# Kernel optimization log

Measured on AMD Instinct MI355X. Metric: run time of the kernel, lower is better.

The kernel has to match this reference:

```python
import jax, jax.numpy as jnp
import numpy as np

B, T, D = 2, 2048, 1024
HEADS = 16
MEM = 512
HEAD_DIM = D // HEADS


def setup_inputs() -> dict:
    key = jax.random.key(0)
    k1, k2, k3, k4, k5 = jax.random.split(key, 5)
    x = jax.random.normal(k1, (B, T, D), dtype=jnp.float32)
    w_qkv = jax.random.normal(k2, (3 * D, D), dtype=jnp.float32) * (1.0 / np.sqrt(D))
    w_out = jax.random.normal(k3, (D, D), dtype=jnp.float32) * (1.0 / np.sqrt(D))
    b_out = jax.random.normal(k4, (D,), dtype=jnp.float32) * 0.01
    memory = jax.random.normal(k5, (MEM, D), dtype=jnp.float32)
    return {"x": x, "w_qkv": w_qkv, "w_out": w_out, "b_out": b_out, "memory": memory}


def reference(x, w_qkv, w_out, b_out, memory):
    b, t, d = x.shape
    h, hd = HEADS, HEAD_DIM
    scale = hd ** -0.5
    # QKV projection: [B,T,3D]
    qkv = jnp.einsum('btd,ed->bte', x, w_qkv)
    q, k, v = jnp.split(qkv, 3, axis=-1)
    # [B,H,T,hd]
    q = q.reshape(b, t, h, hd).transpose(0, 2, 1, 3)
    k = k.reshape(b, t, h, hd).transpose(0, 2, 1, 3)
    v = v.reshape(b, t, h, hd).transpose(0, 2, 1, 3)
    # memory K/V: [B,H,MEM,hd] (broadcast over batch)
    mem = memory.reshape(1, MEM, h, hd).transpose(0, 2, 1, 3)
    mem = jnp.broadcast_to(mem, (b, h, MEM, hd))
    k = jnp.concatenate([mem, k], axis=2)
    v = jnp.concatenate([mem, v], axis=2)
    # attention: scores [B,H,T,MEM+T]
    scores = jnp.einsum('bhqd,bhkd->bhqk', q, k) * scale
    weights = jax.nn.softmax(scores, axis=-1)
    out = jnp.einsum('bhqk,bhkd->bhqd', weights, v)
    out = out.transpose(0, 2, 1, 3).reshape(b, t, d)
    return jnp.einsum('btd,ed->bte', out, w_out) + b_out
```

## Files before the change

kernel.cpp:

```cpp
#include <hip/hip_runtime.h>
#include <hip/hip_bf16.h>
#include <stdint.h>

#define B_   2
#define T_   2048
#define D_   1024
#define H_   16
#define HD_  64
#define MEM_ 512
#define KV_  (MEM_ + T_)
#define NIT_ (KV_ / 64)
#define NIT2_ (NIT_ / 2)

using bf16 = __bf16;
typedef __bf16 bf16x8 __attribute__((ext_vector_type(8)));
typedef float  f32x4  __attribute__((ext_vector_type(4)));
typedef short  s16x4  __attribute__((ext_vector_type(4)));
typedef short  s16x8  __attribute__((ext_vector_type(8)));

__device__ __forceinline__ f32x4 mfma16(bf16x8 a, bf16x8 b, f32x4 c) {
  return __builtin_amdgcn_mfma_f32_16x16x32_bf16(a, b, c, 0, 0, 0);
}

__device__ __forceinline__ void gll16(const void* g, void* l) {
  __builtin_amdgcn_global_load_lds(
      (const __attribute__((address_space(1))) unsigned int*)g,
      (__attribute__((address_space(3))) unsigned int*)l, 16, 0, 0);
}

__device__ __forceinline__ unsigned short bf16_bits(float f) {
  bf16 h = (bf16)f;
  return __builtin_bit_cast(unsigned short, h);
}

__device__ __forceinline__ ushort4 pack4(f32x4 v) {
  ushort4 p;
  p.x = bf16_bits(v[0]); p.y = bf16_bits(v[1]);
  p.z = bf16_bits(v[2]); p.w = bf16_bits(v[3]);
  return p;
}

__device__ __forceinline__ bf16x8 cvt8(f32x4 a, f32x4 b) {
  bf16x8 r;
  r[0] = (bf16)a[0]; r[1] = (bf16)a[1]; r[2] = (bf16)a[2]; r[3] = (bf16)a[3];
  r[4] = (bf16)b[0]; r[5] = (bf16)b[1]; r[6] = (bf16)b[2]; r[7] = (bf16)b[3];
  return r;
}

__device__ __forceinline__ int vperm4(int u) {
  int g = u >> 4, c = (u >> 2) & 3;
  return (g >> 1) * 32 + c * 8 + (g & 1) * 4;
}

__global__ void prep(const float* __restrict__ x, const float* __restrict__ wq,
                     const float* __restrict__ memory,
                     const float* __restrict__ wout,
                     bf16* __restrict__ xb, bf16* __restrict__ wqb,
                     bf16* __restrict__ mem_k, bf16* __restrict__ mem_vt,
                     bf16* __restrict__ wob) {
  int blk = blockIdx.x;
  if (blk < 3584) {
    const float* s = (blk < 2048) ? x : wq;
    bf16* d = (blk < 2048) ? xb : wqb;
    size_t i = ((size_t)(blk < 2048 ? blk : blk - 2048) * 256 + threadIdx.x) * 8;
    f32x4 a = *(const f32x4*)(s + i);
    f32x4 b = *(const f32x4*)(s + i + 4);
    *(bf16x8*)(d + i) = cvt8(a, b);
  } else if (blk < 3840) {
    int idx8 = ((blk - 3584) * 256 + threadIdx.x) * 8;
    int m = idx8 >> 10, d0 = idx8 & 1023;
    int hh = d0 >> 6, hd0 = d0 & 63;
    f32x4 a = *(const f32x4*)(memory + idx8);
    f32x4 b = *(const f32x4*)(memory + idx8 + 4);
    *(bf16x8*)&mem_k[((size_t)hh * MEM_ + m) * HD_ + hd0] = cvt8(a, b);
  } else if (blk < 4096) {
    int idx = (blk - 3840) * 256 + threadIdx.x;
    int d = idx & 1023;
    int m0 = (idx >> 10) * 8;
    bf16x8 r;
#pragma unroll
    for (int j = 0; j < 8; j++)
      r[j] = (bf16)memory[(size_t)(m0 + j) * D_ + d];
    int u = m0 & 63;
    bf16* dst = &mem_vt[(size_t)d * MEM_ + (m0 - u) + vperm4(u)];
    s16x8 rb = __builtin_bit_cast(s16x8, r);
    *(s16x4*)dst = __builtin_shufflevector(rb, rb, 0, 1, 2, 3);
    *(s16x4*)(dst + 8) = __builtin_shufflevector(rb, rb, 4, 5, 6, 7);
  } else {
    size_t i = ((size_t)(blk - 4096) * 256 + threadIdx.x) * 8;
    f32x4 a = *(const f32x4*)(wout + i);
    f32x4 b = *(const f32x4*)(wout + i + 4);
    *(bf16x8*)(wob + i) = cvt8(a, b);
  }
}

__global__ void conv_bf16(const float* __restrict__ s, bf16* __restrict__ d) {
  size_t i = ((size_t)blockIdx.x * 256 + threadIdx.x) * 8;
  f32x4 a = *(const f32x4*)(s + i);
  f32x4 b = *(const f32x4*)(s + i + 4);
  *(bf16x8*)(d + i) = cvt8(a, b);
}

template <int EPI, bool APLANE, int NTILE>
__global__ __launch_bounds__(256, 3) void gemm_bt(
    const bf16* __restrict__ A, const bf16* __restrict__ W,
    const float* __restrict__ bias,
    bf16* __restrict__ q_ws, bf16* __restrict__ k_ws, bf16* __restrict__ vt_ws,
    float* __restrict__ Cout, int K) {
  constexpr int NF = NTILE / 32;
  constexpr int NB = NTILE / 32;
  __shared__ __align__(16) bf16 Als[128 * 64];
  __shared__ __align__(16) bf16 Bls[NTILE * 64];
  char* AB = (char*)Als;
  char* BB = (char*)Bls;
  const int nwg = gridDim.x * gridDim.y;
  int lin = blockIdx.y * gridDim.x + blockIdx.x;
  lin = (lin & 7) * (nwg >> 3) + (lin >> 3);
  const int m0 = (lin / gridDim.x) * 128;
  const int n0 = (lin % gridDim.x) * NTILE;
  const int tid = threadIdx.x;
  const int w = tid >> 6;
  const int lane = tid & 63;
  const int lx = lane & 15;
  const int quad = lane >> 4;
  const int amb = (w & 1) * 64;
  const int bnb = (w >> 1) * (NTILE / 2);
  const int srow = tid >> 3;
  const int cs = (tid & 7) ^ (srow & 7);

  f32x4 acc[4][NF];
#pragma unroll
  for (int i = 0; i < 4; i++)
#pragma unroll
    for (int j = 0; j < NF; j++) acc[i][j] = (f32x4){0.f, 0.f, 0.f, 0.f};

  for (int k0 = 0; k0 < K; k0 += 64) {
    const bf16* pa[4];
#pragma unroll
    for (int g = 0; g < 4; g++) {
      int r = srow + 32 * g;
      if constexpr (APLANE) {
        int hh = k0 >> 6, hd = cs * 8;
        int mA = m0 + r;
        pa[g] = A + ((size_t)((mA >> 11) * H_ + hh) * T_ + (mA & 2047)) * HD_ + hd;
      } else {
        pa[g] = A + (size_t)(m0 + r) * K + k0 + cs * 8;
      }
    }
    const bf16* pb[NB];
#pragma unroll
    for (int g = 0; g < NB; g++)
      pb[g] = W + (size_t)(n0 + srow + 32 * g) * K + k0 + cs * 8;

    __syncthreads();
#pragma unroll
    for (int g = 0; g < 4; g++) gll16(pa[g], AB + g * 4096 + tid * 16);
#pragma unroll
    for (int g = 0; g < NB; g++) gll16(pb[g], BB + g * 4096 + tid * 16);
    __syncthreads();

    bf16x8 af[4][2], bfr[NF][2];
    const int rk = (lx & 7) << 4;
#pragma unroll
    for (int mt = 0; mt < 4; mt++)
#pragma unroll
      for (int kh = 0; kh < 2; kh++)
        af[mt][kh] = *(const bf16x8*)(AB + (size_t)(amb + mt * 16 + lx) * 128 +
                                      ((quad * 16 + kh * 64) ^ rk));
#pragma unroll
    for (int nt = 0; nt < NF; nt++)
#pragma unroll
      for (int kh = 0; kh < 2; kh++)
        bfr[nt][kh] = *(const bf16x8*)(BB + (size_t)(bnb + nt * 16 + lx) * 128 +
                                       ((quad * 16 + kh * 64) ^ rk));
#pragma unroll
    for (int kh = 0; kh < 2; kh++)
#pragma unroll
      for (int mt = 0; mt < 4; mt++)
#pragma unroll
        for (int nt = 0; nt < NF; nt++)
          acc[mt][nt] = mfma16(af[mt][kh], bfr[nt][kh], acc[mt][nt]);
  }

  if (EPI == 0) {
#pragma unroll
    for (int mt = 0; mt < 4; mt++) {
      int mbase = m0 + amb + mt * 16 + quad * 4;
      int b = mbase >> 11;
      int t = mbase & 2047;
#pragma unroll
      for (int nt = 0; nt < NF; nt++) {
        int col = n0 + bnb + nt * 16 + lx;
        int which = col >> 10;
        int d = col & 1023;
        int hh = d >> 6, hdi = d & 63;
        int bh = b * H_ + hh;
        if (which == 0) {
#pragma unroll
          for (int r = 0; r < 4; r++)
            q_ws[((size_t)bh * T_ + t + r) * HD_ + hdi] = (bf16)acc[mt][nt][r];
        } else if (which == 1) {
#pragma unroll
          for (int r = 0; r < 4; r++)
            k_ws[((size_t)bh * T_ + t + r) * HD_ + hdi] = (bf16)acc[mt][nt][r];
        } else {
          int u = t & 63;
          *(ushort4*)&vt_ws[((size_t)bh * HD_ + hdi) * T_ + (t - u) +
                            vperm4(u)] = pack4(acc[mt][nt]);
        }
      }
    }
  } else {
#pragma unroll
    for (int nt = 0; nt < NF; nt++) {
      int col = n0 + bnb + nt * 16 + lx;
      float bias_f = bias[col];
#pragma unroll
      for (int mt = 0; mt < 4; mt++) {
        int mbase = m0 + amb + mt * 16 + quad * 4;
#pragma unroll
        for (int r = 0; r < 4; r++)
          Cout[(size_t)(mbase + r) * D_ + col] = acc[mt][nt][r] + bias_f;
      }
    }
  }
}

__global__ __launch_bounds__(512, 4) void attn_kernel(
    bf16* __restrict__ q_ws, const bf16* __restrict__ k_ws,
    const bf16* __restrict__ vt_ws, const bf16* __restrict__ mem_k,
    const bf16* __restrict__ mem_vt) {
  __shared__ __align__(16) bf16 Kls[2 * 2 * 64 * 64];
  __shared__ __align__(16) bf16 Vls[2 * 2 * 64 * 64];
  char* KB = (char*)Kls;
  char* VB = (char*)Vls;
  const int tid = threadIdx.x;
  const int wh = tid >> 8;
  const int t2 = tid & 255;
  const int w = t2 >> 6;
  const int lane = tid & 63;
  const int lx = lane & 15;
  const int quad = lane >> 4;
  const int bh = blockIdx.x & 31;
  const int qt = blockIdx.x >> 5;
  const int q0 = qt * 128 + w * 32;
  const int h = bh & 15;

  const int srow1 = t2 >> 3;
  const int sc1 = (t2 & 7) ^ (srow1 & 7);

  char* KBh = KB + wh * 16384;
  char* VBh = VB + wh * 16384;

  bf16* qbase = q_ws + ((size_t)bh * T_ + q0) * HD_;

  const bf16* kpl = k_ws + (size_t)bh * T_ * HD_;
  const bf16* vpl = vt_ws + (size_t)bh * HD_ * T_;
  const bf16* mkp = mem_k + (size_t)h * MEM_ * HD_;
  const bf16* mvp = mem_vt + (size_t)h * HD_ * MEM_;

  auto stage = [&](int it2, int bi) {
    const int kv0 = (wh * NIT2_ + it2) * 64;
    const bf16 *kp1, *kp2, *vp1, *vp2;
    if (kv0 < MEM_) {
      kp1 = mkp + (size_t)(kv0 + srow1) * HD_ + sc1 * 8;
      kp2 = kp1 + (size_t)32 * HD_;
      vp1 = mvp + (size_t)srow1 * MEM_ + kv0 + sc1 * 8;
      vp2 = vp1 + (size_t)32 * MEM_;
    } else {
      const int t0 = kv0 - MEM_;
      kp1 = kpl + (size_t)(t0 + srow1) * HD_ + sc1 * 8;
      kp2 = kp1 + (size_t)32 * HD_;
      vp1 = vpl + (size_t)srow1 * T_ + t0 + sc1 * 8;
      vp2 = vp1 + (size_t)32 * T_;
    }
    char* kb = KBh + bi * 8192;
    char* vb = VBh + bi * 8192;
    gll16(kp1, kb + t2 * 16);
    gll16(kp2, kb + t2 * 16 + 4096);
    gll16(vp1, vb + t2 * 16);
    gll16(vp2, vb + t2 * 16 + 4096);
  };

  const float QSCALE = 0.125f * 1.44269504089f;
  bf16x8 qf[2][2];
#pragma unroll
  for (int qg = 0; qg < 2; qg++)
#pragma unroll
    for (int hf = 0; hf < 2; hf++) {
      bf16x8 v = *(const bf16x8*)(qbase + (size_t)(qg * 16 + lx) * HD_ +
                                  hf * 32 + quad * 8);
#pragma unroll
      for (int i = 0; i < 8; i++)
        v[i] = (bf16)((float)v[i] * QSCALE);
      qf[qg][hf] = v;
    }

  bf16x8 ones;
#pragma unroll
  for (int i = 0; i < 8; i++) ones[i] = (bf16)1.0f;

  f32x4 o[4][2];
#pragma unroll
  for (int mt = 0; mt < 4; mt++)
#pragma unroll
    for (int qg = 0; qg < 2; qg++) o[mt][qg] = (f32x4){0.f, 0.f, 0.f, 0.f};
  f32x4 osum[2] = {(f32x4){0.f, 0.f, 0.f, 0.f}, (f32x4){0.f, 0.f, 0.f, 0.f}};

  stage(0, 0);

  for (int it = 0; it < NIT2_; it++) {
    const int cur = it & 1;
    if (it + 1 < NIT2_) {
      stage(it + 1, cur ^ 1);
      asm volatile("s_waitcnt vmcnt(4)" ::: "memory");
    } else {
      asm volatile("s_waitcnt vmcnt(0)" ::: "memory");
    }
    __builtin_amdgcn_s_barrier();
    __builtin_amdgcn_sched_barrier(0);

    const char* KBc = KBh + cur * 8192;
    const char* VBc = VBh + cur * 8192;
    const int sw = (lx & 7) << 4;
    f32x4 s[4][2];
    __builtin_amdgcn_s_setprio(1);
#pragma unroll
    for (int g = 0; g < 4; g++) {
      const char* kb = KBc + (size_t)(g * 16 + lx) * 128;
      bf16x8 ka0 = *(const bf16x8*)(kb + ((quad * 16) ^ sw));
      bf16x8 ka1 = *(const bf16x8*)(kb + ((64 + quad * 16) ^ sw));
#pragma unroll
      for (int qg = 0; qg < 2; qg++) {
        s[g][qg] = (f32x4){0.f, 0.f, 0.f, 0.f};
        s[g][qg] = mfma16(ka0, qf[qg][0], s[g][qg]);
        s[g][qg] = mfma16(ka1, qf[qg][1], s[g][qg]);
      }
    }
    __builtin_amdgcn_s_setprio(0);

    s16x8 pk[2][2];
#pragma unroll
    for (int qg = 0; qg < 2; qg++) {
#pragma unroll
      for (int g = 0; g < 4; g++) {
#pragma unroll
        for (int r = 0; r < 4; r++) {
          float p = __builtin_amdgcn_exp2f(s[g][qg][r]);
          pk[qg][g >> 1][(g & 1) * 4 + r] = (short)bf16_bits(p);
        }
      }
    }

    __builtin_amdgcn_s_setprio(1);
#pragma unroll
    for (int mt = 0; mt < 4; mt++) {
      const char* vb = VBc + (size_t)(mt * 16 + lx) * 128;
#pragma unroll
      for (int p = 0; p < 2; p++) {
        bf16x8 va = *(const bf16x8*)(vb + ((p * 64 + quad * 16) ^ sw));
#pragma unroll
        for (int qg = 0; qg < 2; qg++)
          o[mt][qg] = mfma16(va, __builtin_bit_cast(bf16x8, pk[qg][p]),
                             o[mt][qg]);
      }
    }
#pragma unroll
    for (int p = 0; p < 2; p++)
#pragma unroll
      for (int qg = 0; qg < 2; qg++)
        osum[qg] = mfma16(ones, __builtin_bit_cast(bf16x8, pk[qg][p]),
                          osum[qg]);
    __builtin_amdgcn_s_setprio(0);

    __builtin_amdgcn_sched_barrier(0);
    __builtin_amdgcn_s_barrier();
  }

  float* OS = (float*)KB;
  float* OSS = (float*)VB;
  if (wh == 1) {
    float* dst = OS + t2 * 32;
#pragma unroll
    for (int mt = 0; mt < 4; mt++)
#pragma unroll
      for (int qg = 0; qg < 2; qg++) {
        int c = mt * 2 + qg;
        *(f32x4*)(dst + ((c ^ (t2 & 7)) * 4)) = o[mt][qg];
      }
    OSS[t2 * 2 + 0] = osum[0][0];
    OSS[t2 * 2 + 1] = osum[1][0];
  }
  __syncthreads();
  if (wh == 0) {
    const float* src = OS + t2 * 32;
    float inv[2] = {1.f / (osum[0][0] + OSS[t2 * 2 + 0]),
                    1.f / (osum[1][0] + OSS[t2 * 2 + 1])};
#pragma unroll
    for (int qg = 0; qg < 2; qg++) {
#pragma unroll
      for (int mt = 0; mt < 4; mt++) {
        int c = mt * 2 + qg;
        f32x4 po = *(const f32x4*)(src + ((c ^ (t2 & 7)) * 4));
        f32x4 ov;
#pragma unroll
        for (int r = 0; r < 4; r++) ov[r] = (o[mt][qg][r] + po[r]) * inv[qg];
        *(ushort4*)(qbase + (size_t)(qg * 16 + lx) * HD_ + mt * 16 + quad * 4)
            = pack4(ov);
      }
    }
  }
}

extern "C" void kernel_launch(void* const* d_in, const int* in_sizes, int n_in,
                              void* d_out, int out_size, void* d_ws,
                              size_t ws_size, hipStream_t stream) {
  const float* x      = (const float*)d_in[0];
  const float* w_qkv  = (const float*)d_in[1];
  const float* w_out  = (const float*)d_in[2];
  const float* b_out  = (const float*)d_in[3];
  const float* memory = (const float*)d_in[4];

  char* ws = (char*)d_ws;
  bf16* q_ws   = (bf16*)(ws);
  bf16* k_ws   = (bf16*)(ws + (8u << 20));
  bf16* vt_ws  = (bf16*)(ws + (16u << 20));
  bf16* mem_k  = (bf16*)(ws + (24u << 20));
  bf16* mem_vt = (bf16*)(ws + (25u << 20));
  float* out = (float*)d_out;

  char* outc = (char*)d_out;
  bf16* xb  = (bf16*)(outc);
  bf16* wqb = (bf16*)(outc + (8u << 20));

  const bool big_ws = ws_size >= (28u << 20);
  bf16* wob = big_ws ? (bf16*)(ws + (26u << 20))
                     : (bf16*)(ws + (8u << 20));

  prep<<<dim3(big_ws ? 4608 : 4096), dim3(256), 0, stream>>>(
      x, w_qkv, memory, w_out, xb, wqb, mem_k, mem_vt, wob);
  gemm_bt<0, false, 128><<<dim3(24, 32), dim3(256), 0, stream>>>(
      xb, wqb, nullptr, q_ws, k_ws, vt_ws, nullptr, 1024);
  attn_kernel<<<dim3(512), dim3(512), 0, stream>>>(
      q_ws, k_ws, vt_ws, mem_k, mem_vt);
  if (!big_ws)
    conv_bf16<<<dim3(512), dim3(256), 0, stream>>>(w_out, wob);
  gemm_bt<1, true, 64><<<dim3(16, 32), dim3(256), 0, stream>>>(
      q_ws, wob, b_out, nullptr, nullptr, nullptr, out, 1024);
}
```

Baseline: 180.8 us.

## Add 256x256 double-buffered GEMM kernel for QKV projection

Replaces the 128x128-tile QKV projection GEMM with a new 512-thread kernel using 256x256 tiles and double-buffered LDS staging, so the next K-slice loads while MFMAs run. Larger tiles raise arithmetic intensity and cut global/LDS traffic per FLOP, and setprio boosts the MFMA phase. The trade-off is only 192 workgroups on a large-CU GPU (under one full wave), plus 128KB of LDS per block, which limits occupancy. The old EPI==0 epilogue in gemm_bt is removed since nothing uses it anymore.

```diff
diff --git a/kernel.cpp b/kernel.cpp
--- a/kernel.cpp
+++ b/kernel.cpp
@@ -101,6 +101,122 @@
   *(bf16x8*)(d + i) = cvt8(a, b);
 }
 
+__global__ __launch_bounds__(512, 2) void gemm256(
+    const bf16* __restrict__ A, const bf16* __restrict__ W,
+    bf16* __restrict__ q_ws, bf16* __restrict__ k_ws,
+    bf16* __restrict__ vt_ws, int K) {
+  __shared__ __align__(16) bf16 Als[2 * 256 * 64];
+  __shared__ __align__(16) bf16 Bls[2 * 256 * 64];
+  char* AB = (char*)Als;
+  char* BB = (char*)Bls;
+  const int nwg = gridDim.x * gridDim.y;
+  int lin = blockIdx.y * gridDim.x + blockIdx.x;
+  lin = (lin & 7) * (nwg >> 3) + (lin >> 3);
+  const int m0 = (lin / gridDim.x) * 256;
+  const int n0 = (lin % gridDim.x) * 256;
+  const int tid = threadIdx.x;
+  const int wid = tid >> 6;
+  const int wr = wid >> 2;
+  const int wc = wid & 3;
+  const int lane = tid & 63;
+  const int lx = lane & 15;
+  const int quad = lane >> 4;
+  const int srow = tid >> 3;
+  const int cs = (tid & 7) ^ (srow & 7);
+
+  auto stage = [&](int t, int bi) {
+    const bf16* pa = A + (size_t)(m0 + srow) * K + t * 64 + cs * 8;
+    const bf16* pb = W + (size_t)(n0 + srow) * K + t * 64 + cs * 8;
+    char* ad = AB + bi * 32768 + tid * 16;
+    char* bd = BB + bi * 32768 + tid * 16;
+#pragma unroll
+    for (int g = 0; g < 4; g++) {
+      gll16(pa + (size_t)(g * 64) * K, ad + g * 8192);
+      gll16(pb + (size_t)(g * 64) * K, bd + g * 8192);
+    }
+  };
+
+  f32x4 acc[8][4];
+#pragma unroll
+  for (int m = 0; m < 8; m++)
+#pragma unroll
+    for (int n = 0; n < 4; n++) acc[m][n] = (f32x4){0.f, 0.f, 0.f, 0.f};
+
+  const int rk = (lx & 7) << 4;
+  const int nt_steps = K >> 6;
+
+  stage(0, 0);
+
+  for (int t = 0; t < nt_steps; t++) {
+    const int buf = t & 1;
+    if (t + 1 < nt_steps) {
+      stage(t + 1, buf ^ 1);
+      asm volatile("s_waitcnt vmcnt(8)" ::: "memory");
+    } else {
+      asm volatile("s_waitcnt vmcnt(0)" ::: "memory");
+    }
+    __builtin_amdgcn_s_barrier();
+    __builtin_amdgcn_sched_barrier(0);
+
+    const char* AT = AB + buf * 32768;
+    const char* BT = BB + buf * 32768;
+
+    bf16x8 bfr[4][2];
+#pragma unroll
+    for (int n = 0; n < 4; n++)
+#pragma unroll
+      for (int kh = 0; kh < 2; kh++)
+        bfr[n][kh] = *(const bf16x8*)(BT +
+            (size_t)(wc * 64 + n * 16 + lx) * 128 +
+            ((quad * 16 + kh * 64) ^ rk));
+
+    __builtin_amdgcn_s_setprio(1);
+#pragma unroll
+    for (int m = 0; m < 8; m++) {
+      const char* ar = AT + (size_t)(wr * 128 + m * 16 + lx) * 128;
+      bf16x8 af0 = *(const bf16x8*)(ar + ((quad * 16) ^ rk));
+      bf16x8 af1 = *(const bf16x8*)(ar + ((quad * 16 + 64) ^ rk));
+#pragma unroll
+      for (int n = 0; n < 4; n++) {
+        acc[m][n] = mfma16(af0, bfr[n][0], acc[m][n]);
+        acc[m][n] = mfma16(af1, bfr[n][1], acc[m][n]);
+      }
+    }
+    __builtin_amdgcn_s_setprio(0);
+
+    __builtin_amdgcn_sched_barrier(0);
+    __builtin_amdgcn_s_barrier();
+  }
+
+#pragma unroll
+  for (int m = 0; m < 8; m++) {
+    int mbase = m0 + wr * 128 + m * 16 + quad * 4;
+    int b = mbase >> 11;
+    int tt = mbase & 2047;
+#pragma unroll
+    for (int n = 0; n < 4; n++) {
+      int col = n0 + wc * 64 + n * 16 + lx;
+      int which = col >> 10;
+      int d = col & 1023;
+      int hh = d >> 6, hdi = d & 63;
+      int bh = b * H_ + hh;
+      if (which == 0) {
+#pragma unroll
+        for (int r = 0; r < 4; r++)
+          q_ws[((size_t)bh * T_ + tt + r) * HD_ + hdi] = (bf16)acc[m][n][r];
+      } else if (which == 1) {
+#pragma unroll
+        for (int r = 0; r < 4; r++)
+          k_ws[((size_t)bh * T_ + tt + r) * HD_ + hdi] = (bf16)acc[m][n][r];
+      } else {
+        int u = tt & 63;
+        *(ushort4*)&vt_ws[((size_t)bh * HD_ + hdi) * T_ + (tt - u) +
+                          vperm4(u)] = pack4(acc[m][n]);
+      }
+    }
+  }
+}
+
 template <int EPI, bool APLANE, int NTILE>
 __global__ __launch_bounds__(256, 3) void gemm_bt(
     const bf16* __restrict__ A, const bf16* __restrict__ W,
@@ -183,33 +299,6 @@
   }
 
   if (EPI == 0) {
-#pragma unroll
-    for (int mt = 0; mt < 4; mt++) {
-      int mbase = m0 + amb + mt * 16 + quad * 4;
-      int b = mbase >> 11;
-      int t = mbase & 2047;
-#pragma unroll
-      for (int nt = 0; nt < NF; nt++) {
-        int col = n0 + bnb + nt * 16 + lx;
-        int which = col >> 10;
-        int d = col & 1023;
-        int hh = d >> 6, hdi = d & 63;
-        int bh = b * H_ + hh;
-        if (which == 0) {
-#pragma unroll
-          for (int r = 0; r < 4; r++)
-            q_ws[((size_t)bh * T_ + t + r) * HD_ + hdi] = (bf16)acc[mt][nt][r];
-        } else if (which == 1) {
-#pragma unroll
-          for (int r = 0; r < 4; r++)
-            k_ws[((size_t)bh * T_ + t + r) * HD_ + hdi] = (bf16)acc[mt][nt][r];
-        } else {
-          int u = t & 63;
-          *(ushort4*)&vt_ws[((size_t)bh * HD_ + hdi) * T_ + (t - u) +
-                            vperm4(u)] = pack4(acc[mt][nt]);
-        }
-      }
-    }
   } else {
 #pragma unroll
     for (int nt = 0; nt < NF; nt++) {
@@ -439,8 +528,8 @@
 
   prep<<<dim3(big_ws ? 4608 : 4096), dim3(256), 0, stream>>>(
       x, w_qkv, memory, w_out, xb, wqb, mem_k, mem_vt, wob);
-  gemm_bt<0, false, 128><<<dim3(24, 32), dim3(256), 0, stream>>>(
-      xb, wqb, nullptr, q_ws, k_ws, vt_ws, nullptr, 1024);
+  gemm256<<<dim3(12, 16), dim3(512), 0, stream>>>(
+      xb, wqb, q_ws, k_ws, vt_ws, 1024);
   attn_kernel<<<dim3(512), dim3(512), 0, stream>>>(
       q_ws, k_ws, vt_ws, mem_k, mem_vt);
   if (!big_ws)
```

New measurement: 185.6 us. +2.7%, slower.

## Fuse all stages into one cooperative persistent kernel with grid syncs

Applied to the files above, without the earlier changes.

Replaces the sequence of prep, QKV GEMM, attention and output GEMM launches with a single cooperative kernel of 512 blocks of 512 threads. Stages are separated by grid.sync(), and each block splits into two 256-thread halves that act as independent GEMM teams. The aim is to remove inter-kernel launch gaps and tail drain between stages. In exchange, the GEMMs run with fixed occupancy, and half the block idles during the output GEMM and part of the QKV GEMM. The GEMM inner loop is also reordered so A fragments are loaded per m-tile, which lowers register pressure. If the cooperative launch fails, the code falls back to the old separate-kernel path.

```diff
diff --git a/kernel.cpp b/kernel.cpp
--- a/kernel.cpp
+++ b/kernel.cpp
@@ -1,6 +1,9 @@
 #include <hip/hip_runtime.h>
 #include <hip/hip_bf16.h>
+#include <hip/hip_cooperative_groups.h>
 #include <stdint.h>
+
+namespace cg = cooperative_groups;
 
 #define B_   2
 #define T_   2048
@@ -52,29 +55,28 @@
   return (g >> 1) * 32 + c * 8 + (g & 1) * 4;
 }
 
-__global__ void prep(const float* __restrict__ x, const float* __restrict__ wq,
-                     const float* __restrict__ memory,
-                     const float* __restrict__ wout,
-                     bf16* __restrict__ xb, bf16* __restrict__ wqb,
-                     bf16* __restrict__ mem_k, bf16* __restrict__ mem_vt,
-                     bf16* __restrict__ wob) {
-  int blk = blockIdx.x;
-  if (blk < 3584) {
-    const float* s = (blk < 2048) ? x : wq;
-    bf16* d = (blk < 2048) ? xb : wqb;
-    size_t i = ((size_t)(blk < 2048 ? blk : blk - 2048) * 256 + threadIdx.x) * 8;
+__device__ __forceinline__ void prep_vb(
+    int vb, int t, const float* __restrict__ x, const float* __restrict__ wq,
+    const float* __restrict__ memory, const float* __restrict__ wout,
+    bf16* __restrict__ xb, bf16* __restrict__ wqb,
+    bf16* __restrict__ mem_k, bf16* __restrict__ mem_vt,
+    bf16* __restrict__ wob) {
+  if (vb < 3584) {
+    const float* s = (vb < 2048) ? x : wq;
+    bf16* d = (vb < 2048) ? xb : wqb;
+    size_t i = ((size_t)(vb < 2048 ? vb : vb - 2048) * 256 + t) * 8;
     f32x4 a = *(const f32x4*)(s + i);
     f32x4 b = *(const f32x4*)(s + i + 4);
     *(bf16x8*)(d + i) = cvt8(a, b);
-  } else if (blk < 3840) {
-    int idx8 = ((blk - 3584) * 256 + threadIdx.x) * 8;
+  } else if (vb < 3840) {
+    int idx8 = ((vb - 3584) * 256 + t) * 8;
     int m = idx8 >> 10, d0 = idx8 & 1023;
     int hh = d0 >> 6, hd0 = d0 & 63;
     f32x4 a = *(const f32x4*)(memory + idx8);
     f32x4 b = *(const f32x4*)(memory + idx8 + 4);
     *(bf16x8*)&mem_k[((size_t)hh * MEM_ + m) * HD_ + hd0] = cvt8(a, b);
-  } else if (blk < 4096) {
-    int idx = (blk - 3840) * 256 + threadIdx.x;
+  } else if (vb < 4096) {
+    int idx = (vb - 3840) * 256 + t;
     int d = idx & 1023;
     int m0 = (idx >> 10) * 8;
     bf16x8 r;
@@ -87,46 +89,34 @@
     *(s16x4*)dst = __builtin_shufflevector(rb, rb, 0, 1, 2, 3);
     *(s16x4*)(dst + 8) = __builtin_shufflevector(rb, rb, 4, 5, 6, 7);
   } else {
-    size_t i = ((size_t)(blk - 4096) * 256 + threadIdx.x) * 8;
+    size_t i = ((size_t)(vb - 4096) * 256 + t) * 8;
     f32x4 a = *(const f32x4*)(wout + i);
     f32x4 b = *(const f32x4*)(wout + i + 4);
     *(bf16x8*)(wob + i) = cvt8(a, b);
   }
 }
 
-__global__ void conv_bf16(const float* __restrict__ s, bf16* __restrict__ d) {
-  size_t i = ((size_t)blockIdx.x * 256 + threadIdx.x) * 8;
-  f32x4 a = *(const f32x4*)(s + i);
-  f32x4 b = *(const f32x4*)(s + i + 4);
-  *(bf16x8*)(d + i) = cvt8(a, b);
-}
-
 template <int EPI, bool APLANE, int NTILE>
-__global__ __launch_bounds__(256, 3) void gemm_bt(
+__device__ __forceinline__ void gemm_team(
+    int raw, int lt, char* AB, char* BB,
     const bf16* __restrict__ A, const bf16* __restrict__ W,
     const float* __restrict__ bias,
-    bf16* __restrict__ q_ws, bf16* __restrict__ k_ws, bf16* __restrict__ vt_ws,
-    float* __restrict__ Cout, int K) {
+    bf16* __restrict__ q_ws, bf16* __restrict__ k_ws,
+    bf16* __restrict__ vt_ws, float* __restrict__ Cout,
+    int K, int gx, int nwg) {
   constexpr int NF = NTILE / 32;
   constexpr int NB = NTILE / 32;
-  __shared__ __align__(16) bf16 Als[128 * 64];
-  __shared__ __align__(16) bf16 Bls[NTILE * 64];
-  char* AB = (char*)Als;
-  char* BB = (char*)Bls;
-  const int nwg = gridDim.x * gridDim.y;
-  int lin = blockIdx.y * gridDim.x + blockIdx.x;
-  lin = (lin & 7) * (nwg >> 3) + (lin >> 3);
-  const int m0 = (lin / gridDim.x) * 128;
-  const int n0 = (lin % gridDim.x) * NTILE;
-  const int tid = threadIdx.x;
-  const int w = tid >> 6;
-  const int lane = tid & 63;
+  int lin = (raw & 7) * (nwg >> 3) + (raw >> 3);
+  const int m0 = (lin / gx) * 128;
+  const int n0 = (lin % gx) * NTILE;
+  const int w = lt >> 6;
+  const int lane = lt & 63;
   const int lx = lane & 15;
   const int quad = lane >> 4;
   const int amb = (w & 1) * 64;
   const int bnb = (w >> 1) * (NTILE / 2);
-  const int srow = tid >> 3;
-  const int cs = (tid & 7) ^ (srow & 7);
+  const int srow = lt >> 3;
+  const int cs = (lt & 7) ^ (srow & 7);
 
   f32x4 acc[4][NF];
 #pragma unroll
@@ -154,19 +144,13 @@
 
     __syncthreads();
 #pragma unroll
-    for (int g = 0; g < 4; g++) gll16(pa[g], AB + g * 4096 + tid * 16);
-#pragma unroll
-    for (int g = 0; g < NB; g++) gll16(pb[g], BB + g * 4096 + tid * 16);
+    for (int g = 0; g < 4; g++) gll16(pa[g], AB + g * 4096 + lt * 16);
+#pragma unroll
+    for (int g = 0; g < NB; g++) gll16(pb[g], BB + g * 4096 + lt * 16);
     __syncthreads();
 
-    bf16x8 af[4][2], bfr[NF][2];
+    bf16x8 bfr[NF][2];
     const int rk = (lx & 7) << 4;
-#pragma unroll
-    for (int mt = 0; mt < 4; mt++)
-#pragma unroll
-      for (int kh = 0; kh < 2; kh++)
-        af[mt][kh] = *(const bf16x8*)(AB + (size_t)(amb + mt * 16 + lx) * 128 +
-                                      ((quad * 16 + kh * 64) ^ rk));
 #pragma unroll
     for (int nt = 0; nt < NF; nt++)
 #pragma unroll
@@ -174,12 +158,16 @@
         bfr[nt][kh] = *(const bf16x8*)(BB + (size_t)(bnb + nt * 16 + lx) * 128 +
                                        ((quad * 16 + kh * 64) ^ rk));
 #pragma unroll
-    for (int kh = 0; kh < 2; kh++)
-#pragma unroll
-      for (int mt = 0; mt < 4; mt++)
-#pragma unroll
-        for (int nt = 0; nt < NF; nt++)
-          acc[mt][nt] = mfma16(af[mt][kh], bfr[nt][kh], acc[mt][nt]);
+    for (int mt = 0; mt < 4; mt++) {
+      const char* ar = AB + (size_t)(amb + mt * 16 + lx) * 128;
+      bf16x8 af0 = *(const bf16x8*)(ar + ((quad * 16) ^ rk));
+      bf16x8 af1 = *(const bf16x8*)(ar + ((quad * 16 + 64) ^ rk));
+#pragma unroll
+      for (int nt = 0; nt < NF; nt++) {
+        acc[mt][nt] = mfma16(af0, bfr[nt][0], acc[mt][nt]);
+        acc[mt][nt] = mfma16(af1, bfr[nt][1], acc[mt][nt]);
+      }
+    }
   }
 
   if (EPI == 0) {
@@ -226,23 +214,21 @@
   }
 }
 
-__global__ __launch_bounds__(512, 4) void attn_kernel(
+__device__ __forceinline__ void attn_body(
+    int bx, int tid, char* smem,
     bf16* __restrict__ q_ws, const bf16* __restrict__ k_ws,
     const bf16* __restrict__ vt_ws, const bf16* __restrict__ mem_k,
     const bf16* __restrict__ mem_vt) {
-  __shared__ __align__(16) bf16 Kls[2 * 2 * 64 * 64];
-  __shared__ __align__(16) bf16 Vls[2 * 2 * 64 * 64];
-  char* KB = (char*)Kls;
-  char* VB = (char*)Vls;
-  const int tid = threadIdx.x;
+  char* KB = smem;
+  char* VB = smem + 32768;
   const int wh = tid >> 8;
   const int t2 = tid & 255;
   const int w = t2 >> 6;
   const int lane = tid & 63;
   const int lx = lane & 15;
   const int quad = lane >> 4;
-  const int bh = blockIdx.x & 31;
-  const int qt = blockIdx.x >> 5;
+  const int bh = bx & 31;
+  const int qt = bx >> 5;
   const int q0 = qt * 128 + w * 32;
   const int h = bh & 15;
 
@@ -412,6 +398,97 @@
   }
 }
 
+__global__ __launch_bounds__(512, 4) void fused_all(
+    const float* x, const float* wq, const float* wout, const float* memory,
+    const float* b_out,
+    bf16* xb, bf16* wqb, bf16* mem_k, bf16* mem_vt, bf16* wob,
+    bf16* q_ws, bf16* k_ws, bf16* vt_ws, float* out, int big, int nprep) {
+  __shared__ __align__(16) char smem[65536];
+  const int tid = threadIdx.x;
+  const int half = tid >> 8;
+  const int lt = tid & 255;
+  char* ls = smem + half * 32768;
+  cg::grid_group grid = cg::this_grid();
+
+  for (int vb = blockIdx.x * 2 + half; vb < nprep; vb += 1024)
+    prep_vb(vb, lt, x, wq, memory, wout, xb, wqb, mem_k, mem_vt, wob);
+  grid.sync();
+
+  {
+    int team = (half == 0) ? (int)blockIdx.x
+                           : (blockIdx.x < 256 ? 512 + (int)blockIdx.x : -1);
+    if (team >= 0) {
+      gemm_team<0, false, 128>(team, lt, ls, ls + 16384, xb, wqb, nullptr,
+                               q_ws, k_ws, vt_ws, nullptr, 1024, 24, 768);
+    } else {
+      for (int i = 0; i < 32; i++) __syncthreads();
+    }
+  }
+  grid.sync();
+
+  attn_body(blockIdx.x, tid, smem, q_ws, k_ws, vt_ws, mem_k, mem_vt);
+  grid.sync();
+
+  if (!big) {
+    int gt = blockIdx.x * 512 + tid;
+    if (gt < 131072) {
+      size_t i = (size_t)gt * 8;
+      f32x4 a = *(const f32x4*)(wout + i);
+      f32x4 b = *(const f32x4*)(wout + i + 4);
+      *(bf16x8*)(wob + i) = cvt8(a, b);
+    }
+    grid.sync();
+  }
+
+  {
+    if (half == 0) {
+      gemm_team<1, true, 64>((int)blockIdx.x, lt, ls, ls + 16384, q_ws, wob,
+                             b_out, nullptr, nullptr, nullptr, out,
+                             1024, 16, 512);
+    } else {
+      for (int i = 0; i < 32; i++) __syncthreads();
+    }
+  }
+}
+
+__global__ void prep_k(const float* __restrict__ x, const float* __restrict__ wq,
+                       const float* __restrict__ memory,
+                       const float* __restrict__ wout,
+                       bf16* __restrict__ xb, bf16* __restrict__ wqb,
+                       bf16* __restrict__ mem_k, bf16* __restrict__ mem_vt,
+                       bf16* __restrict__ wob) {
+  prep_vb(blockIdx.x, threadIdx.x, x, wq, memory, wout, xb, wqb,
+          mem_k, mem_vt, wob);
+}
+
+__global__ void conv_bf16(const float* __restrict__ s, bf16* __restrict__ d) {
+  size_t i = ((size_t)blockIdx.x * 256 + threadIdx.x) * 8;
+  f32x4 a = *(const f32x4*)(s + i);
+  f32x4 b = *(const f32x4*)(s + i + 4);
+  *(bf16x8*)(d + i) = cvt8(a, b);
+}
+
+template <int EPI, bool APLANE, int NTILE>
+__global__ __launch_bounds__(256, 3) void gemm_bt(
+    const bf16* __restrict__ A, const bf16* __restrict__ W,
+    const float* __restrict__ bias,
+    bf16* __restrict__ q_ws, bf16* __restrict__ k_ws, bf16* __restrict__ vt_ws,
+    float* __restrict__ Cout, int K) {
+  __shared__ __align__(16) char ts[16384 + NTILE * 128];
+  gemm_team<EPI, APLANE, NTILE>(
+      blockIdx.y * gridDim.x + blockIdx.x, threadIdx.x, ts, ts + 16384,
+      A, W, bias, q_ws, k_ws, vt_ws, Cout, K, gridDim.x,
+      gridDim.x * gridDim.y);
+}
+
+__global__ __launch_bounds__(512, 4) void attn_kernel(
+    bf16* __restrict__ q_ws, const bf16* __restrict__ k_ws,
+    const bf16* __restrict__ vt_ws, const bf16* __restrict__ mem_k,
+    const bf16* __restrict__ mem_vt) {
+  __shared__ __align__(16) char smem[65536];
+  attn_body(blockIdx.x, threadIdx.x, smem, q_ws, k_ws, vt_ws, mem_k, mem_vt);
+}
+
 extern "C" void kernel_launch(void* const* d_in, const int* in_sizes, int n_in,
                               void* d_out, int out_size, void* d_ws,
                               size_t ws_size, hipStream_t stream) {
@@ -437,14 +514,29 @@
   bf16* wob = big_ws ? (bf16*)(ws + (26u << 20))
                      : (bf16*)(ws + (8u << 20));
 
-  prep<<<dim3(big_ws ? 4608 : 4096), dim3(256), 0, stream>>>(
-      x, w_qkv, memory, w_out, xb, wqb, mem_k, mem_vt, wob);
-  gemm_bt<0, false, 128><<<dim3(24, 32), dim3(256), 0, stream>>>(
-      xb, wqb, nullptr, q_ws, k_ws, vt_ws, nullptr, 1024);
-  attn_kernel<<<dim3(512), dim3(512), 0, stream>>>(
-      q_ws, k_ws, vt_ws, mem_k, mem_vt);
-  if (!big_ws)
-    conv_bf16<<<dim3(512), dim3(256), 0, stream>>>(w_out, wob);
-  gemm_bt<1, true, 64><<<dim3(16, 32), dim3(256), 0, stream>>>(
-      q_ws, wob, b_out, nullptr, nullptr, nullptr, out, 1024);
-}
+  int bigi = big_ws ? 1 : 0;
+  int nprep = big_ws ? 4608 : 4096;
+
+  void* kargs[] = {
+      (void*)&x, (void*)&w_qkv, (void*)&w_out, (void*)&memory, (void*)&b_out,
+      (void*)&xb, (void*)&wqb, (void*)&mem_k, (void*)&mem_vt, (void*)&wob,
+      (void*)&q_ws, (void*)&k_ws, (void*)&vt_ws, (void*)&out,
+      (void*)&bigi, (void*)&nprep};
+
+  hipError_t err = hipLaunchCooperativeKernel(
+      (const void*)fused_all, dim3(512), dim3(512), kargs, 0, stream);
+
+  if (err != hipSuccess) {
+    (void)hipGetLastError();
+    prep_k<<<dim3(nprep), dim3(256), 0, stream>>>(
+        x, w_qkv, memory, w_out, xb, wqb, mem_k, mem_vt, wob);
+    gemm_bt<0, false, 128><<<dim3(24, 32), dim3(256), 0, stream>>>(
+        xb, wqb, nullptr, q_ws, k_ws, vt_ws, nullptr, 1024);
+    attn_kernel<<<dim3(512), dim3(512), 0, stream>>>(
+        q_ws, k_ws, vt_ws, mem_k, mem_vt);
+    if (!big_ws)
+      conv_bf16<<<dim3(512), dim3(256), 0, stream>>>(w_out, wob);
+    gemm_bt<1, true, 64><<<dim3(16, 32), dim3(256), 0, stream>>>(
+        q_ws, wob, b_out, nullptr, nullptr, nullptr, out, 1024);
+  }
+}
```

New measurement: 379.1 us. +109.7%, slower.
